# Kernel optimization log

Hardware: AMD Instinct MI355X
Metric: run time of the kernel (lower is better)

## Reference

```python
import jax, jax.numpy as jnp
import numpy as np

B, S, D = 2, 2048, 1024
H = 16
HD = D // H  # 64


def setup_inputs() -> dict:
    key = jax.random.key(0)
    k1, k2, k3, k4, k5, k6 = jax.random.split(key, 6)
    hidden_states = jax.random.normal(k1, (B, S, D), dtype=jnp.float32)
    attention_mask = jax.random.randint(k2, (B, S), 0, 2, dtype=jnp.int32)
    scale = 1.0 / np.sqrt(D)
    Wq = jax.random.normal(k3, (D, D), dtype=jnp.float32) * scale
    bq = jax.random.normal(k4, (D,), dtype=jnp.float32) * 0.02
    Wk = jax.random.normal(k5, (D, D), dtype=jnp.float32) * scale
    bk = jax.random.normal(k6, (D,), dtype=jnp.float32) * 0.02
    return {"hidden_states": hidden_states, "attention_mask": attention_mask,
            "Wq": Wq, "bq": bq, "Wk": Wk, "bk": bk}


def _split_heads(x):
    # [B, S, D] -> [B, H, S, HD]
    b, s, _ = x.shape
    return x.reshape(b, s, H, HD).transpose(0, 2, 1, 3)


def reference(hidden_states, attention_mask, Wq, bq, Wk, bk):
    dh = jnp.sqrt(jnp.float32(HD))
    q = _split_heads(hidden_states @ Wq + bq)            # [B,H,S,HD]
    k = _split_heads(hidden_states @ Wk + bk)            # [B,H,S,HD]
    v = q + k                                            # value = Q + K
    k_t = -jax.nn.log_sigmoid(-k)                        # negate the logsigmoid(-K) transform
    scores = jnp.einsum('bhqd,bhkd->bhqk', q, k_t) / dh  # [B,H,S,S]
    # mask applied on the QUERY axis (dim 2), broadcast over key axis (faithful to source)
    mask = (attention_mask[:, None, :, None] == 0)       # [B,1,S,1]
    scores = jnp.where(mask, jnp.float32(-10000.0), scores)
    probs = jax.nn.softmax(scores, axis=-1)              # dropout: eval mode (identity)
    ctx = jnp.einsum('bhqk,bhkd->bhqd', probs, v)        # [B,H,S,HD]
    ctx = ctx.transpose(0, 2, 1, 3).reshape(B, S, D)
    return ctx
```

## Files before the change

kernel.cpp:

```cpp
#include <hip/hip_runtime.h>
#include <hip/hip_bf16.h>

#define B_ 2
#define S_ 2048
#define D_ 1024
#define H_ 16
#define HD_ 64

typedef __attribute__((ext_vector_type(8))) short short8;
typedef __attribute__((ext_vector_type(4))) short short4v;
typedef __attribute__((ext_vector_type(4))) float float4v;

typedef const __attribute__((address_space(1))) void* gas_ptr;
typedef __attribute__((address_space(3))) void* las_ptr;

static __device__ inline void gl_lds16(const void* g, void* l) {
  __builtin_amdgcn_global_load_lds((gas_ptr)g, (las_ptr)l, 16, 0, 0);
}

static __device__ inline float b2f(__hip_bfloat16 h) { return __bfloat162float(h); }

static __device__ inline short f2bs(float x) {
  __hip_bfloat16 h = __float2bfloat16(x);
  union { __hip_bfloat16 h; short s; } u; u.h = h; return u.s;
}
static __device__ inline float bs2f(short s) {
  union { short s; __hip_bfloat16 h; } u; u.s = s; return __bfloat162float(u.h);
}

static __device__ inline float4v mfma32(short8 a, short8 b, float4v c) {
  return __builtin_amdgcn_mfma_f32_16x16x32_bf16(a, b, c, 0, 0, 0);
}
static __device__ inline float4v mfma16(short4v a, short4v b, float4v c) {
  return __builtin_amdgcn_mfma_f32_16x16x16bf16_1k(a, b, c, 0, 0, 0);
}

__global__ __launch_bounds__(256) void pre(
    const float* __restrict__ Wq, const float* __restrict__ Wk,
    const float* __restrict__ hs,
    __hip_bfloat16* __restrict__ Wqt, __hip_bfloat16* __restrict__ Wkt,
    __hip_bfloat16* __restrict__ hsb) {
  if (blockIdx.z == 2) {
    const int blk = blockIdx.y * 16 + blockIdx.x;
    for (int it = 0; it < 8; ++it) {
      const size_t i = (size_t)blk * 16384 + it * 2048 + threadIdx.x * 8;
      const float4v v0 = *(const float4v*)(hs + i);
      const float4v v1 = *(const float4v*)(hs + i + 4);
      short8 s;
      for (int j = 0; j < 4; ++j) { s[j] = f2bs(v0[j]); s[4 + j] = f2bs(v1[j]); }
      *(short8*)(hsb + i) = s;
    }
    return;
  }
  const float* W = blockIdx.z ? Wk : Wq;
  __hip_bfloat16* Wt = blockIdx.z ? Wkt : Wqt;
  __shared__ float t[64][65];
  const int n0 = blockIdx.x * 64, k0 = blockIdx.y * 64;
  const int c = threadIdx.x & 63, r0 = threadIdx.x >> 6;
  for (int i = 0; i < 16; ++i) {
    const int r = i * 4 + r0;
    t[c][r] = W[(size_t)(k0 + r) * D_ + n0 + c];
  }
  __syncthreads();
  for (int i = 0; i < 16; ++i) {
    const int rr = i * 4 + r0;
    Wt[(size_t)(n0 + rr) * D_ + k0 + c] = __float2bfloat16(t[rr][c]);
  }
}

__global__ __launch_bounds__(256) void gemm_fused(
    const __hip_bfloat16* __restrict__ A,
    const __hip_bfloat16* __restrict__ Wqt, const __hip_bfloat16* __restrict__ Wkt,
    const float* __restrict__ bq, const float* __restrict__ bk,
    __hip_bfloat16* __restrict__ q_out, __hip_bfloat16* __restrict__ kt_out,
    __hip_bfloat16* __restrict__ vT) {
  const int n0 = blockIdx.x * 128, m0 = blockIdx.y * 64;
  __shared__ __hip_bfloat16 As[2][64 * 32];
  __shared__ __hip_bfloat16 Bq[2][128 * 32];
  __shared__ __hip_bfloat16 Bk[2][128 * 32];
  const int tid = threadIdx.x, wid = tid >> 6, lane = tid & 63;
  const int wm = (wid >> 1) * 32, wn = (wid & 1) * 64;
  const int l15 = lane & 15, l4 = lane >> 4;
  const float4v zz = {0.f, 0.f, 0.f, 0.f};
  float4v accq[2][4], acck[2][4];
  for (int i = 0; i < 2; ++i)
    for (int j = 0; j < 4; ++j) { accq[i][j] = zz; acck[i][j] = zz; }
  const int arow = wid * 16 + (lane >> 2);
  const int brow = wid * 32 + (lane >> 2);
  const int lk8 = (lane & 3) * 8;
  gl_lds16(A + (size_t)(m0 + arow) * D_ + lk8, As[0] + wid * 512);
  gl_lds16(Wqt + (size_t)(n0 + brow) * D_ + lk8, Bq[0] + wid * 1024);
  gl_lds16(Wqt + (size_t)(n0 + brow + 16) * D_ + lk8, Bq[0] + wid * 1024 + 512);
  gl_lds16(Wkt + (size_t)(n0 + brow) * D_ + lk8, Bk[0] + wid * 1024);
  gl_lds16(Wkt + (size_t)(n0 + brow + 16) * D_ + lk8, Bk[0] + wid * 1024 + 512);
  int p = 0;
  for (int kb = 0; kb < 32; ++kb) {
    __syncthreads();
    if (kb < 31) {
      const int kc = (kb + 1) * 32 + lk8;
      gl_lds16(A + (size_t)(m0 + arow) * D_ + kc, As[p ^ 1] + wid * 512);
      gl_lds16(Wqt + (size_t)(n0 + brow) * D_ + kc, Bq[p ^ 1] + wid * 1024);
      gl_lds16(Wqt + (size_t)(n0 + brow + 16) * D_ + kc, Bq[p ^ 1] + wid * 1024 + 512);
      gl_lds16(Wkt + (size_t)(n0 + brow) * D_ + kc, Bk[p ^ 1] + wid * 1024);
      gl_lds16(Wkt + (size_t)(n0 + brow + 16) * D_ + kc, Bk[p ^ 1] + wid * 1024 + 512);
    }
    short8 af[2], bfq[4], bfk[4];
    const int fo = l4 * 8;
    for (int rt = 0; rt < 2; ++rt)
      af[rt] = *(const short8*)(As[p] + (wm + rt * 16 + l15) * 32 + fo);
    for (int ct = 0; ct < 4; ++ct) {
      bfq[ct] = *(const short8*)(Bq[p] + (wn + ct * 16 + l15) * 32 + fo);
      bfk[ct] = *(const short8*)(Bk[p] + (wn + ct * 16 + l15) * 32 + fo);
    }
    for (int rt = 0; rt < 2; ++rt)
      for (int ct = 0; ct < 4; ++ct) {
        accq[rt][ct] = mfma32(af[rt], bfq[ct], accq[rt][ct]);
        acck[rt][ct] = mfma32(af[rt], bfk[ct], acck[rt][ct]);
      }
    p ^= 1;
  }
  float bvq[4], bvk[4];
  for (int ct = 0; ct < 4; ++ct) {
    bvq[ct] = bq[n0 + wn + ct * 16 + l15];
    bvk[ct] = bk[n0 + wn + ct * 16 + l15];
  }
  for (int rt = 0; rt < 2; ++rt)
    for (int ct = 0; ct < 4; ++ct) {
      const int col = n0 + wn + ct * 16 + l15;
      const int h = col >> 6, d = col & 63;
      const int rowb = m0 + wm + rt * 16 + l4 * 4;
      short4v vv;
      for (int r = 0; r < 4; ++r) {
        const int row = rowb + r;
        const float qv = accq[rt][ct][r] + bvq[ct];
        const float kv = acck[rt][ct][r] + bvk[ct];
        const float sp = fmaxf(kv, 0.f) + __logf(1.f + __expf(-fabsf(kv)));
        q_out[(size_t)row * D_ + col] = __float2bfloat16(qv);
        kt_out[(size_t)row * D_ + col] = __float2bfloat16(sp);
        vv[r] = f2bs(qv + kv);
      }
      const int b = rowb >> 11, s = rowb & 2047;
      *(short4v*)(vT + ((size_t)(b * H_ + h) * HD_ + d) * S_ + s) = vv;
    }
}

#define KP 72
__global__ __launch_bounds__(512, 4) void attn(
    const __hip_bfloat16* __restrict__ qb, const __hip_bfloat16* __restrict__ ktb,
    const __hip_bfloat16* __restrict__ vT, const int* __restrict__ mask,
    float* __restrict__ out) {
  __shared__ __hip_bfloat16 smem[2][4 * 64 * KP];
  const int q0 = blockIdx.x * 128, h = blockIdx.y, b = blockIdx.z;
  const int tid = threadIdx.x, wid = tid >> 6, lane = tid & 63;
  const int l15 = lane & 15, l4 = lane >> 4;
  const int hf = wid >> 2, qt = wid & 3;
  const __hip_bfloat16* qh = qb + (size_t)b * S_ * D_ + h * HD_;
  const __hip_bfloat16* kh = ktb + (size_t)b * S_ * D_ + h * HD_;
  const __hip_bfloat16* vh = vT + (size_t)(b * H_ + h) * HD_ * S_;
  const int srow = (tid & 255) >> 2;
  const int scol = (tid & 3) * 8;
  const int koff = hf * 64 * KP;
  const int voff = (2 + hf) * 64 * KP;

  const int qlA = qt * 32 + l15, qlB = qlA + 16;
  const int qrA = q0 + qlA, qrB = q0 + qlB;
  const float mqA = (mask[b * S_ + qrA] != 0) ? 0.125f : 0.f;
  const float mqB = (mask[b * S_ + qrB] != 0) ? 0.125f : 0.f;
  const short8 rA0 = *(const short8*)(qh + (size_t)qrA * D_ + l4 * 8);
  const short8 rA1 = *(const short8*)(qh + (size_t)qrA * D_ + 32 + l4 * 8);
  const short8 rB0 = *(const short8*)(qh + (size_t)qrB * D_ + l4 * 8);
  const short8 rB1 = *(const short8*)(qh + (size_t)qrB * D_ + 32 + l4 * 8);
  short8 bqA0, bqA1, bqB0, bqB1;
  for (int j = 0; j < 8; ++j) {
    bqA0[j] = f2bs(bs2f(rA0[j]) * mqA);
    bqA1[j] = f2bs(bs2f(rA1[j]) * mqA);
    bqB0[j] = f2bs(bs2f(rB0[j]) * mqB);
    bqB1[j] = f2bs(bs2f(rB1[j]) * mqB);
  }

  const float4v zz = {0.f, 0.f, 0.f, 0.f};
  float4v oaccA[4] = {zz, zz, zz, zz};
  float4v oaccB[4] = {zz, zz, zz, zz};
  float lsumA = 0.f, lsumB = 0.f;

  const int kb0 = hf * 1024;
  short8 gk0 = *(const short8*)(kh + (size_t)(kb0 + srow) * D_ + scol);
  short8 gk1 = *(const short8*)(kh + (size_t)(kb0 + srow) * D_ + scol + 32);
  short8 gv0 = *(const short8*)(vh + (size_t)srow * S_ + kb0 + scol);
  short8 gv1 = *(const short8*)(vh + (size_t)srow * S_ + kb0 + scol + 32);

  int p = 0;
  for (int c = 0; c < 16; ++c) {
    *(short8*)&smem[p][koff + srow * KP + scol] = gk0;
    *(short8*)&smem[p][koff + srow * KP + scol + 32] = gk1;
    *(short8*)&smem[p][voff + srow * KP + scol] = gv0;
    *(short8*)&smem[p][voff + srow * KP + scol + 32] = gv1;
    __syncthreads();
    if (c < 15) {
      const int kb = hf * 1024 + (c + 1) * 64;
      gk0 = *(const short8*)(kh + (size_t)(kb + srow) * D_ + scol);
      gk1 = *(const short8*)(kh + (size_t)(kb + srow) * D_ + scol + 32);
      gv0 = *(const short8*)(vh + (size_t)srow * S_ + kb + scol);
      gv1 = *(const short8*)(vh + (size_t)srow * S_ + kb + scol + 32);
    }
    const __hip_bfloat16* kb_ = &smem[p][koff];
    const __hip_bfloat16* vb_ = &smem[p][voff];
#pragma unroll
    for (int t = 0; t < 4; ++t) {
      const short8 ak0 = *(const short8*)&kb_[(t * 16 + l15) * KP + l4 * 8];
      const short8 ak1 = *(const short8*)&kb_[(t * 16 + l15) * KP + 32 + l4 * 8];
      float4v cA = zz, cB = zz;
      cA = mfma32(ak0, bqA0, cA);
      cA = mfma32(ak1, bqA1, cA);
      cB = mfma32(ak0, bqB0, cB);
      cB = mfma32(ak1, bqB1, cB);
      short4v pA, pB;
#pragma unroll
      for (int r = 0; r < 4; ++r) {
        const float eA = __expf(cA[r]); lsumA += eA; pA[r] = f2bs(eA);
        const float eB = __expf(cB[r]); lsumB += eB; pB[r] = f2bs(eB);
      }
#pragma unroll
      for (int dt = 0; dt < 4; ++dt) {
        const short4v av = *(const short4v*)&vb_[(dt * 16 + l15) * KP + t * 16 + l4 * 4];
        oaccA[dt] = mfma16(av, pA, oaccA[dt]);
        oaccB[dt] = mfma16(av, pB, oaccB[dt]);
      }
    }
    p ^= 1;
  }
  float lA = lsumA + __shfl_xor(lsumA, 16); lA += __shfl_xor(lA, 32);
  float lB = lsumB + __shfl_xor(lsumB, 16); lB += __shfl_xor(lB, 32);
  __syncthreads();
  float* mbuf = (float*)&smem[0][0];
  float* mlb = (float*)&smem[0][0] + 128 * 68;
  if (hf == 1) {
#pragma unroll
    for (int dt = 0; dt < 4; ++dt)
#pragma unroll
      for (int r = 0; r < 4; ++r) {
        mbuf[qlA * 68 + dt * 16 + l4 * 4 + r] = oaccA[dt][r];
        mbuf[qlB * 68 + dt * 16 + l4 * 4 + r] = oaccB[dt][r];
      }
    if (l4 == 0) { mlb[qlA] = lA; mlb[qlB] = lB; }
  }
  __syncthreads();
  if (hf == 0) {
    const float liA = 1.f / (lA + mlb[qlA]);
    const float liB = 1.f / (lB + mlb[qlB]);
#pragma unroll
    for (int dt = 0; dt < 4; ++dt) {
      const float4v pa = *(const float4v*)&mbuf[qlA * 68 + dt * 16 + l4 * 4];
      const float4v pb = *(const float4v*)&mbuf[qlB * 68 + dt * 16 + l4 * 4];
      float4v va, vb;
#pragma unroll
      for (int r = 0; r < 4; ++r) {
        va[r] = (oaccA[dt][r] + pa[r]) * liA;
        vb[r] = (oaccB[dt][r] + pb[r]) * liB;
      }
      *(float4v*)(out + (size_t)(b * S_ + qrA) * D_ + h * HD_ + dt * 16 + l4 * 4) = va;
      *(float4v*)(out + (size_t)(b * S_ + qrB) * D_ + h * HD_ + dt * 16 + l4 * 4) = vb;
    }
  }
}

extern "C" void kernel_launch(void* const* d_in, const int* in_sizes, int n_in,
                              void* d_out, int out_size, void* d_ws, size_t ws_size,
                              hipStream_t stream) {
  const float* hs = (const float*)d_in[0];
  const int* mask = (const int*)d_in[1];
  const float* Wq = (const float*)d_in[2];
  const float* bq = (const float*)d_in[3];
  const float* Wk = (const float*)d_in[4];
  const float* bk = (const float*)d_in[5];
  float* out = (float*)d_out;
  char* ws = (char*)d_ws;
  const size_t MB = 1u << 20;
  __hip_bfloat16* q_b = (__hip_bfloat16*)(ws + 0 * MB);
  __hip_bfloat16* k_b = (__hip_bfloat16*)(ws + 8 * MB);
  __hip_bfloat16* hsb = (__hip_bfloat16*)(ws + 16 * MB);
  __hip_bfloat16* vT  = (__hip_bfloat16*)(ws + 24 * MB);
  __hip_bfloat16* Wqt = (__hip_bfloat16*)(ws + 32 * MB);
  __hip_bfloat16* Wkt = (__hip_bfloat16*)(ws + 34 * MB);

  pre<<<dim3(16, 16, 3), 256, 0, stream>>>(Wq, Wk, hs, Wqt, Wkt, hsb);
  gemm_fused<<<dim3(8, 64), 256, 0, stream>>>(hsb, Wqt, Wkt, bq, bk, q_b, k_b, vT);
  attn<<<dim3(16, 16, 2), 512, 0, stream>>>(q_b, k_b, vT, mask, out);
}
```

Baseline: 178.9 us.

## Read swizzled V directly from global memory and switch softmax to exp2

The projection kernel now stores V^T with a swizzled sequence index, so each lane can load 16 contiguous values matching the MFMA A-operand order for four key sub-tiles. The attention kernel drops V staging through shared memory, halving LDS use, and raises the occupancy hint from 4 to 6 blocks per SM. The 1/sqrt(d) scale is folded together with log2(e) so the kernel can use the hardware exp2, and probabilities are packed with paired bf16 conversions. The risk is that V loads now come uncached-through-LDS straight from global/L2 inside the inner loop, which may add latency, and the higher occupancy target may cause register spills.

```diff
diff --git a/kernel.cpp b/kernel.cpp
--- a/kernel.cpp
+++ b/kernel.cpp
@@ -26,6 +26,12 @@
 }
 static __device__ inline float bs2f(short s) {
   union { short s; __hip_bfloat16 h; } u; u.s = s; return __bfloat162float(u.h);
+}
+static __device__ inline short4v pk4(float a, float b, float c, float d) {
+  union { __hip_bfloat162 h[2]; short4v s; } u;
+  u.h[0] = __float22bfloat162_rn(float2{a, b});
+  u.h[1] = __float22bfloat162_rn(float2{c, d});
+  return u.s;
 }
 
 static __device__ inline float4v mfma32(short8 a, short8 b, float4v c) {
@@ -140,16 +146,17 @@
         vv[r] = f2bs(qv + kv);
       }
       const int b = rowb >> 11, s = rowb & 2047;
-      *(short4v*)(vT + ((size_t)(b * H_ + h) * HD_ + d) * S_ + s) = vv;
+      const int sw = (s & ~63) | (((s >> 2) & 3) << 4) | (((s >> 4) & 3) << 2);
+      *(short4v*)(vT + ((size_t)(b * H_ + h) * HD_ + d) * S_ + sw) = vv;
     }
 }
 
 #define KP 72
-__global__ __launch_bounds__(512, 4) void attn(
+__global__ __launch_bounds__(512, 6) void attn(
     const __hip_bfloat16* __restrict__ qb, const __hip_bfloat16* __restrict__ ktb,
     const __hip_bfloat16* __restrict__ vT, const int* __restrict__ mask,
     float* __restrict__ out) {
-  __shared__ __hip_bfloat16 smem[2][4 * 64 * KP];
+  __shared__ __hip_bfloat16 smem[2][2 * 64 * KP];
   const int q0 = blockIdx.x * 128, h = blockIdx.y, b = blockIdx.z;
   const int tid = threadIdx.x, wid = tid >> 6, lane = tid & 63;
   const int l15 = lane & 15, l4 = lane >> 4;
@@ -160,12 +167,12 @@
   const int srow = (tid & 255) >> 2;
   const int scol = (tid & 3) * 8;
   const int koff = hf * 64 * KP;
-  const int voff = (2 + hf) * 64 * KP;
 
   const int qlA = qt * 32 + l15, qlB = qlA + 16;
   const int qrA = q0 + qlA, qrB = q0 + qlB;
-  const float mqA = (mask[b * S_ + qrA] != 0) ? 0.125f : 0.f;
-  const float mqB = (mask[b * S_ + qrB] != 0) ? 0.125f : 0.f;
+  const float SC = 0.125f * 1.44269504f;
+  const float mqA = (mask[b * S_ + qrA] != 0) ? SC : 0.f;
+  const float mqB = (mask[b * S_ + qrB] != 0) ? SC : 0.f;
   const short8 rA0 = *(const short8*)(qh + (size_t)qrA * D_ + l4 * 8);
   const short8 rA1 = *(const short8*)(qh + (size_t)qrA * D_ + 32 + l4 * 8);
   const short8 rB0 = *(const short8*)(qh + (size_t)qrB * D_ + l4 * 8);
@@ -186,25 +193,20 @@
   const int kb0 = hf * 1024;
   short8 gk0 = *(const short8*)(kh + (size_t)(kb0 + srow) * D_ + scol);
   short8 gk1 = *(const short8*)(kh + (size_t)(kb0 + srow) * D_ + scol + 32);
-  short8 gv0 = *(const short8*)(vh + (size_t)srow * S_ + kb0 + scol);
-  short8 gv1 = *(const short8*)(vh + (size_t)srow * S_ + kb0 + scol + 32);
 
   int p = 0;
   for (int c = 0; c < 16; ++c) {
     *(short8*)&smem[p][koff + srow * KP + scol] = gk0;
     *(short8*)&smem[p][koff + srow * KP + scol + 32] = gk1;
-    *(short8*)&smem[p][voff + srow * KP + scol] = gv0;
-    *(short8*)&smem[p][voff + srow * KP + scol + 32] = gv1;
     __syncthreads();
     if (c < 15) {
       const int kb = hf * 1024 + (c + 1) * 64;
       gk0 = *(const short8*)(kh + (size_t)(kb + srow) * D_ + scol);
       gk1 = *(const short8*)(kh + (size_t)(kb + srow) * D_ + scol + 32);
-      gv0 = *(const short8*)(vh + (size_t)srow * S_ + kb + scol);
-      gv1 = *(const short8*)(vh + (size_t)srow * S_ + kb + scol + 32);
     }
     const __hip_bfloat16* kb_ = &smem[p][koff];
-    const __hip_bfloat16* vb_ = &smem[p][voff];
+    const __hip_bfloat16* vrow0 = vh + kb0 + c * 64;
+    short4v pA[4], pB[4];
 #pragma unroll
     for (int t = 0; t < 4; ++t) {
       const short8 ak0 = *(const short8*)&kb_[(t * 16 + l15) * KP + l4 * 8];
@@ -214,18 +216,32 @@
       cA = mfma32(ak1, bqA1, cA);
       cB = mfma32(ak0, bqB0, cB);
       cB = mfma32(ak1, bqB1, cB);
-      short4v pA, pB;
+      float eA[4], eB[4];
 #pragma unroll
       for (int r = 0; r < 4; ++r) {
-        const float eA = __expf(cA[r]); lsumA += eA; pA[r] = f2bs(eA);
-        const float eB = __expf(cB[r]); lsumB += eB; pB[r] = f2bs(eB);
-      }
-#pragma unroll
-      for (int dt = 0; dt < 4; ++dt) {
-        const short4v av = *(const short4v*)&vb_[(dt * 16 + l15) * KP + t * 16 + l4 * 4];
-        oaccA[dt] = mfma16(av, pA, oaccA[dt]);
-        oaccB[dt] = mfma16(av, pB, oaccB[dt]);
-      }
+        eA[r] = __builtin_amdgcn_exp2f(cA[r]); lsumA += eA[r];
+        eB[r] = __builtin_amdgcn_exp2f(cB[r]); lsumB += eB[r];
+      }
+      pA[t] = pk4(eA[0], eA[1], eA[2], eA[3]);
+      pB[t] = pk4(eB[0], eB[1], eB[2], eB[3]);
+    }
+#pragma unroll
+    for (int dt = 0; dt < 4; ++dt) {
+      const __hip_bfloat16* vr = vrow0 + (size_t)(dt * 16 + l15) * S_ + l4 * 16;
+      const short8 av0 = *(const short8*)vr;
+      const short8 av1 = *(const short8*)(vr + 8);
+      const short4v a0 = {av0[0], av0[1], av0[2], av0[3]};
+      const short4v a1 = {av0[4], av0[5], av0[6], av0[7]};
+      const short4v a2 = {av1[0], av1[1], av1[2], av1[3]};
+      const short4v a3 = {av1[4], av1[5], av1[6], av1[7]};
+      oaccA[dt] = mfma16(a0, pA[0], oaccA[dt]);
+      oaccB[dt] = mfma16(a0, pB[0], oaccB[dt]);
+      oaccA[dt] = mfma16(a1, pA[1], oaccA[dt]);
+      oaccB[dt] = mfma16(a1, pB[1], oaccB[dt]);
+      oaccA[dt] = mfma16(a2, pA[2], oaccA[dt]);
+      oaccB[dt] = mfma16(a2, pB[2], oaccB[dt]);
+      oaccA[dt] = mfma16(a3, pA[3], oaccA[dt]);
+      oaccB[dt] = mfma16(a3, pB[3], oaccB[dt]);
     }
     p ^= 1;
   }
```

Result: slower. 388.0 us (+116.8%).

## Give each attention wave a full key sweep over 16 queries instead of split-K

Applied to the files above, without the earlier changes.

The attention kernel no longer splits the key range across two wave groups, each group covering 32 queries per wave. Each of the 8 waves now owns 16 query rows and loops over all 32 key tiles, with a smaller shared tile and the launch bound raised from 4 to 8 blocks per CU for higher occupancy. The log2(e) factor is folded into the query scale so it can use the exp2 intrinsic, and probabilities are packed to bf16 in pairs. Output is staged through shared memory so rows are written out coalesced. The trade-off is that each K fragment read from LDS now feeds one query tile instead of two, which doubles LDS reads per MFMA.

```diff
diff --git a/kernel.cpp b/kernel.cpp
--- a/kernel.cpp
+++ b/kernel.cpp
@@ -26,6 +26,12 @@
 }
 static __device__ inline float bs2f(short s) {
   union { short s; __hip_bfloat16 h; } u; u.s = s; return __bfloat162float(u.h);
+}
+static __device__ inline short4v pk4(float a, float b, float c, float d) {
+  union { __hip_bfloat162 h[2]; short4v s; } u;
+  u.h[0] = __float22bfloat162_rn(float2{a, b});
+  u.h[1] = __float22bfloat162_rn(float2{c, d});
+  return u.s;
 }
 
 static __device__ inline float4v mfma32(short8 a, short8 b, float4v c) {
@@ -145,122 +151,92 @@
 }
 
 #define KP 72
-__global__ __launch_bounds__(512, 4) void attn(
+__global__ __launch_bounds__(512, 8) void attn(
     const __hip_bfloat16* __restrict__ qb, const __hip_bfloat16* __restrict__ ktb,
     const __hip_bfloat16* __restrict__ vT, const int* __restrict__ mask,
     float* __restrict__ out) {
-  __shared__ __hip_bfloat16 smem[2][4 * 64 * KP];
+  __shared__ __hip_bfloat16 smem[2][2 * 64 * KP];
   const int q0 = blockIdx.x * 128, h = blockIdx.y, b = blockIdx.z;
   const int tid = threadIdx.x, wid = tid >> 6, lane = tid & 63;
   const int l15 = lane & 15, l4 = lane >> 4;
-  const int hf = wid >> 2, qt = wid & 3;
   const __hip_bfloat16* qh = qb + (size_t)b * S_ * D_ + h * HD_;
   const __hip_bfloat16* kh = ktb + (size_t)b * S_ * D_ + h * HD_;
   const __hip_bfloat16* vh = vT + (size_t)(b * H_ + h) * HD_ * S_;
-  const int srow = (tid & 255) >> 2;
-  const int scol = (tid & 3) * 8;
-  const int koff = hf * 64 * KP;
-  const int voff = (2 + hf) * 64 * KP;
-
-  const int qlA = qt * 32 + l15, qlB = qlA + 16;
-  const int qrA = q0 + qlA, qrB = q0 + qlB;
-  const float mqA = (mask[b * S_ + qrA] != 0) ? 0.125f : 0.f;
-  const float mqB = (mask[b * S_ + qrB] != 0) ? 0.125f : 0.f;
-  const short8 rA0 = *(const short8*)(qh + (size_t)qrA * D_ + l4 * 8);
-  const short8 rA1 = *(const short8*)(qh + (size_t)qrA * D_ + 32 + l4 * 8);
-  const short8 rB0 = *(const short8*)(qh + (size_t)qrB * D_ + l4 * 8);
-  const short8 rB1 = *(const short8*)(qh + (size_t)qrB * D_ + 32 + l4 * 8);
-  short8 bqA0, bqA1, bqB0, bqB1;
+  const int voff = 64 * KP;
+  const int srow = tid >> 3;
+  const int scol = (tid & 7) * 8;
+
+  const int ql = wid * 16 + l15;
+  const int qr = q0 + ql;
+  const float SC = 0.125f * 1.44269504f;
+  const float mq = (mask[b * S_ + qr] != 0) ? SC : 0.f;
+  const short8 rq0 = *(const short8*)(qh + (size_t)qr * D_ + l4 * 8);
+  const short8 rq1 = *(const short8*)(qh + (size_t)qr * D_ + 32 + l4 * 8);
+  short8 bq0, bq1;
   for (int j = 0; j < 8; ++j) {
-    bqA0[j] = f2bs(bs2f(rA0[j]) * mqA);
-    bqA1[j] = f2bs(bs2f(rA1[j]) * mqA);
-    bqB0[j] = f2bs(bs2f(rB0[j]) * mqB);
-    bqB1[j] = f2bs(bs2f(rB1[j]) * mqB);
+    bq0[j] = f2bs(bs2f(rq0[j]) * mq);
+    bq1[j] = f2bs(bs2f(rq1[j]) * mq);
   }
 
   const float4v zz = {0.f, 0.f, 0.f, 0.f};
-  float4v oaccA[4] = {zz, zz, zz, zz};
-  float4v oaccB[4] = {zz, zz, zz, zz};
-  float lsumA = 0.f, lsumB = 0.f;
-
-  const int kb0 = hf * 1024;
-  short8 gk0 = *(const short8*)(kh + (size_t)(kb0 + srow) * D_ + scol);
-  short8 gk1 = *(const short8*)(kh + (size_t)(kb0 + srow) * D_ + scol + 32);
-  short8 gv0 = *(const short8*)(vh + (size_t)srow * S_ + kb0 + scol);
-  short8 gv1 = *(const short8*)(vh + (size_t)srow * S_ + kb0 + scol + 32);
+  float4v oacc[4] = {zz, zz, zz, zz};
+  float lsum = 0.f;
+
+  short8 gk = *(const short8*)(kh + (size_t)srow * D_ + scol);
+  short8 gv = *(const short8*)(vh + (size_t)srow * S_ + scol);
 
   int p = 0;
-  for (int c = 0; c < 16; ++c) {
-    *(short8*)&smem[p][koff + srow * KP + scol] = gk0;
-    *(short8*)&smem[p][koff + srow * KP + scol + 32] = gk1;
-    *(short8*)&smem[p][voff + srow * KP + scol] = gv0;
-    *(short8*)&smem[p][voff + srow * KP + scol + 32] = gv1;
+  for (int c = 0; c < 32; ++c) {
+    *(short8*)&smem[p][srow * KP + scol] = gk;
+    *(short8*)&smem[p][voff + srow * KP + scol] = gv;
     __syncthreads();
-    if (c < 15) {
-      const int kb = hf * 1024 + (c + 1) * 64;
-      gk0 = *(const short8*)(kh + (size_t)(kb + srow) * D_ + scol);
-      gk1 = *(const short8*)(kh + (size_t)(kb + srow) * D_ + scol + 32);
-      gv0 = *(const short8*)(vh + (size_t)srow * S_ + kb + scol);
-      gv1 = *(const short8*)(vh + (size_t)srow * S_ + kb + scol + 32);
-    }
-    const __hip_bfloat16* kb_ = &smem[p][koff];
+    if (c < 31) {
+      const int kb = (c + 1) * 64;
+      gk = *(const short8*)(kh + (size_t)(kb + srow) * D_ + scol);
+      gv = *(const short8*)(vh + (size_t)srow * S_ + kb + scol);
+    }
+    const __hip_bfloat16* kb_ = &smem[p][0];
     const __hip_bfloat16* vb_ = &smem[p][voff];
 #pragma unroll
     for (int t = 0; t < 4; ++t) {
       const short8 ak0 = *(const short8*)&kb_[(t * 16 + l15) * KP + l4 * 8];
       const short8 ak1 = *(const short8*)&kb_[(t * 16 + l15) * KP + 32 + l4 * 8];
-      float4v cA = zz, cB = zz;
-      cA = mfma32(ak0, bqA0, cA);
-      cA = mfma32(ak1, bqA1, cA);
-      cB = mfma32(ak0, bqB0, cB);
-      cB = mfma32(ak1, bqB1, cB);
-      short4v pA, pB;
-#pragma unroll
-      for (int r = 0; r < 4; ++r) {
-        const float eA = __expf(cA[r]); lsumA += eA; pA[r] = f2bs(eA);
-        const float eB = __expf(cB[r]); lsumB += eB; pB[r] = f2bs(eB);
-      }
+      float4v cc = zz;
+      cc = mfma32(ak0, bq0, cc);
+      cc = mfma32(ak1, bq1, cc);
+      float e[4];
+#pragma unroll
+      for (int r = 0; r < 4; ++r) { e[r] = __builtin_amdgcn_exp2f(cc[r]); lsum += e[r]; }
+      const short4v pf = pk4(e[0], e[1], e[2], e[3]);
 #pragma unroll
       for (int dt = 0; dt < 4; ++dt) {
         const short4v av = *(const short4v*)&vb_[(dt * 16 + l15) * KP + t * 16 + l4 * 4];
-        oaccA[dt] = mfma16(av, pA, oaccA[dt]);
-        oaccB[dt] = mfma16(av, pB, oaccB[dt]);
+        oacc[dt] = mfma16(av, pf, oacc[dt]);
       }
     }
     p ^= 1;
   }
-  float lA = lsumA + __shfl_xor(lsumA, 16); lA += __shfl_xor(lA, 32);
-  float lB = lsumB + __shfl_xor(lsumB, 16); lB += __shfl_xor(lB, 32);
+  float l = lsum + __shfl_xor(lsum, 16); l += __shfl_xor(l, 32);
   __syncthreads();
   float* mbuf = (float*)&smem[0][0];
   float* mlb = (float*)&smem[0][0] + 128 * 68;
-  if (hf == 1) {
-#pragma unroll
-    for (int dt = 0; dt < 4; ++dt)
-#pragma unroll
-      for (int r = 0; r < 4; ++r) {
-        mbuf[qlA * 68 + dt * 16 + l4 * 4 + r] = oaccA[dt][r];
-        mbuf[qlB * 68 + dt * 16 + l4 * 4 + r] = oaccB[dt][r];
-      }
-    if (l4 == 0) { mlb[qlA] = lA; mlb[qlB] = lB; }
-  }
+  #pragma unroll
+  for (int dt = 0; dt < 4; ++dt)
+#pragma unroll
+    for (int r = 0; r < 4; ++r)
+      mbuf[ql * 68 + dt * 16 + l4 * 4 + r] = oacc[dt][r];
+  if (l4 == 0) mlb[ql] = l;
   __syncthreads();
-  if (hf == 0) {
-    const float liA = 1.f / (lA + mlb[qlA]);
-    const float liB = 1.f / (lB + mlb[qlB]);
-#pragma unroll
-    for (int dt = 0; dt < 4; ++dt) {
-      const float4v pa = *(const float4v*)&mbuf[qlA * 68 + dt * 16 + l4 * 4];
-      const float4v pb = *(const float4v*)&mbuf[qlB * 68 + dt * 16 + l4 * 4];
-      float4v va, vb;
-#pragma unroll
-      for (int r = 0; r < 4; ++r) {
-        va[r] = (oaccA[dt][r] + pa[r]) * liA;
-        vb[r] = (oaccB[dt][r] + pb[r]) * liB;
-      }
-      *(float4v*)(out + (size_t)(b * S_ + qrA) * D_ + h * HD_ + dt * 16 + l4 * 4) = va;
-      *(float4v*)(out + (size_t)(b * S_ + qrB) * D_ + h * HD_ + dt * 16 + l4 * 4) = vb;
-    }
+  const int qq = wid * 16 + (lane >> 2);
+  const int dg = (lane & 3) * 16;
+  const float li = 1.f / mlb[qq];
+  float* orow = out + (size_t)(b * S_ + q0 + qq) * D_ + h * HD_ + dg;
+#pragma unroll
+  for (int i = 0; i < 4; ++i) {
+    float4v v = *(const float4v*)&mbuf[qq * 68 + dg + i * 4];
+#pragma unroll
+    for (int r = 0; r < 4; ++r) v[r] *= li;
+    *(float4v*)(orow + i * 4) = v;
   }
 }
 
```

Result: no change. 176.0 us (-1.7%).
